# Kernel tuning notes

Hardware: AMD Instinct MI355X
Metric: run time of the kernel (lower is better)

Reference implementation:

```python
import jax, jax.numpy as jnp
import numpy as np

B, F, E = 4096, 39, 16
FIELD_DIMS = [1000] * F
OFFSETS = jnp.asarray(np.concatenate([[0], np.cumsum(FIELD_DIMS)[:-1]]).astype(np.int64))
I_IDX, J_IDX = np.triu_indices(F, 1)  # 741 pairs (i<j)
I_IDX = jnp.asarray(I_IDX); J_IDX = jnp.asarray(J_IDX)
MLP_DIMS = [2 * 741 * E, 400, 400, 400]
EPS = 1e-5


def setup_inputs() -> dict:
    key = jax.random.key(0)
    ks = jax.random.split(key, 20)
    s = 0.02
    inp = {
        'x': jax.random.randint(ks[0], (B, F), 0, 1000, dtype=jnp.int64),
        'emb': jax.random.normal(ks[1], (sum(FIELD_DIMS), E), jnp.float32) * s,
        'sen_w1': jax.random.normal(ks[2], (F, F), jnp.float32) * s,
        'sen_b1': jnp.zeros((F,), jnp.float32),
        'sen_w2': jax.random.normal(ks[3], (F, F), jnp.float32) * s,
        'sen_b2': jnp.zeros((F,), jnp.float32),
        'Wb1': jax.random.normal(ks[4], (E, E), jnp.float32) * s,
        'Wb2': jax.random.normal(ks[5], (E, E), jnp.float32) * s,
    }
    for li in range(3):
        din, dout = MLP_DIMS[li], MLP_DIMS[li + 1]
        inp[f'mw{li}'] = jax.random.normal(ks[6 + li], (dout, din), jnp.float32) * s
        inp[f'mb{li}'] = jnp.zeros((dout,), jnp.float32)
        inp[f'g{li}'] = jnp.ones((dout,), jnp.float32)
        inp[f'be{li}'] = jnp.zeros((dout,), jnp.float32)
    inp['mw3'] = jax.random.normal(ks[9], (1, MLP_DIMS[-1]), jnp.float32) * s
    inp['mb3'] = jnp.zeros((1,), jnp.float32)
    return inp


def _bilinear_all(v, W):
    # v: [B,F,E]; p_ij = (v_i W^T) * v_j for all i<j -> [B, P*E]
    proj = jnp.einsum('bfe,de->bfd', v, W)
    p = proj[:, I_IDX] * v[:, J_IDX]  # [B, 741, E]
    return p.reshape(v.shape[0], -1)


def _bn(h, g, be):
    mu = h.mean(axis=0)
    var = h.var(axis=0)
    return g * (h - mu) * jax.lax.rsqrt(var + EPS) + be


def _forward(x, emb, sen_w1, sen_b1, sen_w2, sen_b2, Wb1, Wb2,
             mw0, mb0, g0, be0, mw1, mb1, g1, be1, mw2, mb2, g2, be2, mw3, mb3):
    xe = emb[x + OFFSETS[None, :]]  # [B,F,E]
    # SENet: max over embed dim, two-layer excitation with ReLU
    z = jnp.max(xe, axis=2)  # [B,F]
    a = jax.nn.relu(jax.nn.relu(z @ sen_w1.T + sen_b1) @ sen_w2.T + sen_b2)  # [B,F]
    x_sen = a[:, :, None] * xe
    x_con = jnp.concatenate([_bilinear_all(xe, Wb1), _bilinear_all(x_sen, Wb2)], axis=1)
    h = x_con
    for w, b, g, be in ((mw0, mb0, g0, be0), (mw1, mb1, g1, be1), (mw2, mb2, g2, be2)):
        h = jax.nn.relu(_bn(h @ w.T + b, g, be))  # dropout = identity (eval)
    return h @ mw3.T + mb3  # [B,1]


def reference(x, emb, sen_w1, sen_b1, sen_w2, sen_b2, Wb1, Wb2,
              mw0, mb0, g0, be0, mw1, mb1, g1, be1, mw2, mb2, g2, be2, mw3, mb3):
    return _forward(x, emb, sen_w1, sen_b1, sen_w2, sen_b2, Wb1, Wb2,
                    mw0, mb0, g0, be0, mw1, mb1, g1, be1, mw2, mb2, g2, be2, mw3, mb3)
```

## Files before the change

### kernel.cpp

```cpp
#include <hip/hip_runtime.h>
#include <stdint.h>

#define B_ROWS  4096
#define F_FIELDS 39
#define NPAIR   741
#define XCON_K  23712
#define KP      23744
#define NP      512
#define HID     400
#define SPLITK0 8
#define KITERS0 (KP/64)

#define OFF_XCON 0ull
#define SZ_XCON  ((size_t)B_ROWS * KP * 2)
#define OFF_W0B  (OFF_XCON + SZ_XCON)
#define SZ_W0B   ((size_t)NP * KP * 2)
#define OFF_W1B  (OFF_W0B + SZ_W0B)
#define SZ_WSM   ((size_t)NP * NP * 2)
#define OFF_W2B  (OFF_W1B + SZ_WSM)
#define OFF_HPRE (OFF_W2B + SZ_WSM)
#define SZ_HPRE  ((size_t)B_ROWS * NP * 4)
#define OFF_HN   (OFF_HPRE + SZ_HPRE)
#define SZ_HN    ((size_t)B_ROWS * NP * 2)
#define OFF_STATS (OFF_HN + SZ_HN)
#define WS_NEEDED (OFF_STATS + 8192)

__device__ __forceinline__ unsigned short f2bf(float f) {
    union { float f; unsigned u; } v; v.f = f;
    unsigned r = (v.u + 0x7FFFu + ((v.u >> 16) & 1u)) >> 16;
    return (unsigned short)r;
}
__device__ __forceinline__ float bf2f(unsigned short h) {
    union { unsigned u; float f; } v; v.u = ((unsigned)h) << 16;
    return v.f;
}
__device__ __forceinline__ void gl_lds16(const void* g, void* l) {
    __builtin_amdgcn_global_load_lds(
        (const __attribute__((address_space(1))) void*)g,
        (__attribute__((address_space(3))) void*)l, 16, 0, 0);
}

typedef __bf16 bf16x8 __attribute__((ext_vector_type(8)));
typedef float  floatx4 __attribute__((ext_vector_type(4)));

__global__ __launch_bounds__(256) void build_xcon(
    const int* __restrict__ x, const float* __restrict__ emb,
    const float* __restrict__ w1, const float* __restrict__ b1,
    const float* __restrict__ w2, const float* __restrict__ b2,
    const float* __restrict__ Wb1, const float* __restrict__ Wb2,
    unsigned short* __restrict__ xcon)
{
    __shared__ float xe[624], pp[2][624];
    __shared__ float zz[40], tt[40], aa[40];
    __shared__ short itab[NPAIR], jtab[NPAIR];
    const int b = blockIdx.x, tid = threadIdx.x;

    for (int p = tid; p < NPAIR; p += 256) {
        int i = 0, s = 0;
        while (p >= s + (F_FIELDS - 1 - i)) { s += F_FIELDS - 1 - i; ++i; }
        itab[p] = (short)i;
        jtab[p] = (short)(i + 1 + (p - s));
    }
    if (tid < 156) {
        int f = tid >> 2, e4 = (tid & 3) * 4;
        int row = x[b * F_FIELDS + f] + 1000 * f;
        *(float4*)&xe[f * 16 + e4] = *(const float4*)&emb[row * 16 + e4];
    }
    __syncthreads();
    if (tid < F_FIELDS) {
        float m = xe[tid * 16];
        for (int e = 1; e < 16; ++e) m = fmaxf(m, xe[tid * 16 + e]);
        zz[tid] = m;
    }
    __syncthreads();
    if (tid < F_FIELDS) {
        float s = b1[tid];
        for (int g = 0; g < F_FIELDS; ++g) s += zz[g] * w1[tid * F_FIELDS + g];
        tt[tid] = fmaxf(s, 0.f);
    }
    __syncthreads();
    if (tid < F_FIELDS) {
        float s = b2[tid];
        for (int g = 0; g < F_FIELDS; ++g) s += tt[g] * w2[tid * F_FIELDS + g];
        aa[tid] = fmaxf(s, 0.f);
    }
    __syncthreads();
    for (int idx = tid; idx < 624; idx += 256) {
        int f = idx >> 4, d = idx & 15;
        float s1 = 0.f, s2 = 0.f;
        for (int e = 0; e < 16; ++e) {
            float v = xe[f * 16 + e];
            s1 += v * Wb1[d * 16 + e];
            s2 += v * Wb2[d * 16 + e];
        }
        pp[0][idx] = s1; pp[1][idx] = s2;
    }
    __syncthreads();
    unsigned short* out = xcon + (size_t)b * KP;
    for (int c = tid; c < 1484; c += 256) {
        if (c < 2 * NPAIR) {
            const int half = (c >= NPAIR);
            const int p = c - NPAIR * half;
            const int i = itab[p], j = jtab[p];
            const float f = half ? aa[i] * aa[j] : 1.f;
            const float* pr = &pp[half][i * 16];
            const float* xr = &xe[j * 16];
            unsigned short u[16];
#pragma unroll
            for (int e = 0; e < 16; ++e) u[e] = f2bf(f * pr[e] * xr[e]);
            uint4 v0, v1;
            v0.x = u[0] | ((unsigned)u[1] << 16);  v0.y = u[2] | ((unsigned)u[3] << 16);
            v0.z = u[4] | ((unsigned)u[5] << 16);  v0.w = u[6] | ((unsigned)u[7] << 16);
            v1.x = u[8] | ((unsigned)u[9] << 16);  v1.y = u[10] | ((unsigned)u[11] << 16);
            v1.z = u[12] | ((unsigned)u[13] << 16); v1.w = u[14] | ((unsigned)u[15] << 16);
            uint4* dst = (uint4*)(out + (half ? 11856 : 0) + p * 16);
            dst[0] = v0; dst[1] = v1;
        } else {
            uint4 z; z.x = z.y = z.z = z.w = 0u;
            ((uint4*)(out + XCON_K))[c - 2 * NPAIR] = z;
        }
    }
}

__global__ __launch_bounds__(256) void cvt_w0(const float* __restrict__ w, unsigned short* __restrict__ o_) {
    const int o = blockIdx.x;
    for (int k4 = threadIdx.x; k4 < KP / 4; k4 += 256) {
        const int k = k4 * 4;
        unsigned short u[4] = {0, 0, 0, 0};
        if (o < HID && k < XCON_K) {
            float4 v = *(const float4*)&w[(size_t)o * XCON_K + k];
            u[0] = f2bf(v.x); u[1] = f2bf(v.y); u[2] = f2bf(v.z); u[3] = f2bf(v.w);
        }
        uint2 pk; pk.x = u[0] | ((unsigned)u[1] << 16); pk.y = u[2] | ((unsigned)u[3] << 16);
        *(uint2*)&o_[(size_t)o * KP + k] = pk;
    }
}
__global__ __launch_bounds__(256) void cvt_wsm(const float* __restrict__ wa, const float* __restrict__ wb,
                                               unsigned short* __restrict__ oa, unsigned short* __restrict__ ob) {
    const int which = blockIdx.x >> 9;
    const int o = blockIdx.x & 511;
    const float* w = which ? wb : wa;
    unsigned short* o_ = which ? ob : oa;
    for (int k = threadIdx.x; k < NP; k += 256) {
        float v = (o < HID && k < HID) ? w[o * HID + k] : 0.f;
        o_[o * NP + k] = f2bf(v);
    }
}

__global__ __launch_bounds__(256, 2) void gemm0(
    const unsigned short* __restrict__ A, const unsigned short* __restrict__ Bm,
    float* __restrict__ C, int kcnt)
{
    __shared__ __align__(16) unsigned short As[128 * 64];
    __shared__ __align__(16) unsigned short Bs[256 * 64];
    const int tid = threadIdx.x;
    const int m0 = blockIdx.y * 128, n0 = blockIdx.x * 256;
    int kb = blockIdx.z * kcnt;
    int ke = kb + kcnt; if (ke > KITERS0) ke = KITERS0;

    const unsigned short* Ag = A + (size_t)(m0 + (tid >> 3)) * KP + ((tid & 7) * 8);
    const unsigned short* Bg = Bm + (size_t)(n0 + (tid >> 3)) * KP + ((tid & 7) * 8);
    unsigned short* Asl = As + tid * 8;
    unsigned short* Bsl = Bs + tid * 8;

    const int wv = tid >> 6, ln = tid & 63;
    const int wm = (wv >> 1) * 64, wn = (wv & 1) * 128;
    const int l15 = ln & 15, lq = ln >> 4;

    floatx4 acc[4][8];
#pragma unroll
    for (int mi = 0; mi < 4; ++mi)
#pragma unroll
        for (int ni = 0; ni < 8; ++ni)
            acc[mi][ni] = (floatx4){0.f, 0.f, 0.f, 0.f};

    for (int kt = kb; kt < ke; ++kt) {
        const size_t ko = (size_t)kt * 64;
#pragma unroll
        for (int i = 0; i < 4; ++i)
            gl_lds16(Ag + (size_t)(i * 32) * KP + ko, Asl + i * 2048);
#pragma unroll
        for (int i = 0; i < 8; ++i)
            gl_lds16(Bg + (size_t)(i * 32) * KP + ko, Bsl + i * 2048);
        __syncthreads();
#pragma unroll
        for (int kk = 0; kk < 64; kk += 32) {
            bf16x8 af[4], bfr[8];
#pragma unroll
            for (int t = 0; t < 4; ++t)
                af[t] = *(const bf16x8*)(As + (wm + t * 16 + l15) * 64 + kk + lq * 8);
#pragma unroll
            for (int t = 0; t < 8; ++t)
                bfr[t] = *(const bf16x8*)(Bs + (wn + t * 16 + l15) * 64 + kk + lq * 8);
#pragma unroll
            for (int mi = 0; mi < 4; ++mi)
#pragma unroll
                for (int ni = 0; ni < 8; ++ni)
                    acc[mi][ni] = __builtin_amdgcn_mfma_f32_16x16x32_bf16(
                        af[mi], bfr[ni], acc[mi][ni], 0, 0, 0);
        }
        __syncthreads();
    }
#pragma unroll
    for (int mi = 0; mi < 4; ++mi)
#pragma unroll
        for (int ni = 0; ni < 8; ++ni) {
            const int col = n0 + wn + ni * 16 + l15;
            const int row0 = m0 + wm + mi * 16 + lq * 4;
#pragma unroll
            for (int r = 0; r < 4; ++r)
                atomicAdd(&C[(size_t)(row0 + r) * NP + col], acc[mi][ni][r]);
        }
}

__global__ __launch_bounds__(256) void gemm_small(
    const unsigned short* __restrict__ A, const unsigned short* __restrict__ Bm,
    float* __restrict__ C)
{
    __shared__ __align__(16) unsigned short As[64 * 64];
    __shared__ __align__(16) unsigned short Bs[128 * 64];
    const int tid = threadIdx.x;
    const int m0 = blockIdx.y * 64, n0 = blockIdx.x * 128;

    const unsigned short* Ag = A + (size_t)(m0 + (tid >> 3)) * NP + ((tid & 7) * 8);
    const unsigned short* Bg = Bm + (size_t)(n0 + (tid >> 3)) * NP + ((tid & 7) * 8);
    unsigned short* Asl = As + tid * 8;
    unsigned short* Bsl = Bs + tid * 8;

    const int wv = tid >> 6, ln = tid & 63;
    const int wm = (wv >> 1) * 32, wn = (wv & 1) * 64;
    const int l15 = ln & 15, lq = ln >> 4;

    floatx4 acc[2][4];
#pragma unroll
    for (int mi = 0; mi < 2; ++mi)
#pragma unroll
        for (int ni = 0; ni < 4; ++ni)
            acc[mi][ni] = (floatx4){0.f, 0.f, 0.f, 0.f};

    for (int kt = 0; kt < NP / 64; ++kt) {
        const size_t ko = (size_t)kt * 64;
#pragma unroll
        for (int i = 0; i < 2; ++i)
            gl_lds16(Ag + (size_t)(i * 32) * NP + ko, Asl + i * 2048);
#pragma unroll
        for (int i = 0; i < 4; ++i)
            gl_lds16(Bg + (size_t)(i * 32) * NP + ko, Bsl + i * 2048);
        __syncthreads();
#pragma unroll
        for (int kk = 0; kk < 64; kk += 32) {
            bf16x8 af[2], bfr[4];
#pragma unroll
            for (int t = 0; t < 2; ++t)
                af[t] = *(const bf16x8*)(As + (wm + t * 16 + l15) * 64 + kk + lq * 8);
#pragma unroll
            for (int t = 0; t < 4; ++t)
                bfr[t] = *(const bf16x8*)(Bs + (wn + t * 16 + l15) * 64 + kk + lq * 8);
#pragma unroll
            for (int mi = 0; mi < 2; ++mi)
#pragma unroll
                for (int ni = 0; ni < 4; ++ni)
                    acc[mi][ni] = __builtin_amdgcn_mfma_f32_16x16x32_bf16(
                        af[mi], bfr[ni], acc[mi][ni], 0, 0, 0);
        }
        __syncthreads();
    }
#pragma unroll
    for (int mi = 0; mi < 2; ++mi)
#pragma unroll
        for (int ni = 0; ni < 4; ++ni) {
            const int col = n0 + wn + ni * 16 + l15;
            const int row0 = m0 + wm + mi * 16 + lq * 4;
#pragma unroll
            for (int r = 0; r < 4; ++r)
                C[(size_t)(row0 + r) * NP + col] = acc[mi][ni][r];
        }
}

__global__ __launch_bounds__(256) void colstats(const float* __restrict__ H,
                                                float* __restrict__ cs, float* __restrict__ csq) {
    const int tid = threadIdx.x;
    const int c4 = (tid & 127) * 4;
    const int ro = tid >> 7;
    const int r0 = blockIdx.x * 32;
    float s0 = 0, s1 = 0, s2 = 0, s3 = 0, q0 = 0, q1 = 0, q2 = 0, q3 = 0;
#pragma unroll
    for (int i = 0; i < 16; ++i) {
        float4 v = *(const float4*)&H[(size_t)(r0 + ro + 2 * i) * NP + c4];
        s0 += v.x; q0 += v.x * v.x;  s1 += v.y; q1 += v.y * v.y;
        s2 += v.z; q2 += v.z * v.z;  s3 += v.w; q3 += v.w * v.w;
    }
    atomicAdd(&cs[c4], s0); atomicAdd(&cs[c4 + 1], s1);
    atomicAdd(&cs[c4 + 2], s2); atomicAdd(&cs[c4 + 3], s3);
    atomicAdd(&csq[c4], q0); atomicAdd(&csq[c4 + 1], q1);
    atomicAdd(&csq[c4 + 2], q2); atomicAdd(&csq[c4 + 3], q3);
}

__global__ __launch_bounds__(256) void bnrelu(const float* __restrict__ H,
                       const float* __restrict__ cs, const float* __restrict__ csq,
                       const float* __restrict__ g, const float* __restrict__ be,
                       unsigned short* __restrict__ O) {
    __shared__ float sc[NP], sh[NP];
    for (int c = threadIdx.x; c < NP; c += 256) {
        float mean = cs[c] * (1.f / 4096.f);
        float var  = csq[c] * (1.f / 4096.f) - mean * mean;
        float s = (c < HID ? g[c] : 0.f) * rsqrtf(var + 1e-5f);
        sc[c] = s;
        sh[c] = (c < HID ? be[c] : 0.f) - mean * s;
    }
    __syncthreads();
    const size_t n4 = (size_t)B_ROWS * NP / 4;
    const size_t stride = (size_t)gridDim.x * 256;
    for (size_t i = (size_t)blockIdx.x * 256 + threadIdx.x; i < n4; i += stride) {
        const int c = (int)(i & 127) * 4;
        float4 v = ((const float4*)H)[i];
        unsigned short u0 = f2bf(fmaxf(v.x * sc[c]     + sh[c],     0.f));
        unsigned short u1 = f2bf(fmaxf(v.y * sc[c + 1] + sh[c + 1], 0.f));
        unsigned short u2 = f2bf(fmaxf(v.z * sc[c + 2] + sh[c + 2], 0.f));
        unsigned short u3 = f2bf(fmaxf(v.w * sc[c + 3] + sh[c + 3], 0.f));
        uint2 pk; pk.x = u0 | ((unsigned)u1 << 16); pk.y = u2 | ((unsigned)u3 << 16);
        *(uint2*)&O[i * 4] = pk;
    }
}

__global__ void final_dot(const unsigned short* __restrict__ H, const float* __restrict__ w,
                          const float* __restrict__ b, float* __restrict__ out) {
    const int row = blockIdx.x, ln = threadIdx.x;
    const unsigned short* h = H + (size_t)row * NP;
    float s = 0.f;
    for (int c = ln; c < HID; c += 64) s += bf2f(h[c]) * w[c];
    for (int o = 32; o; o >>= 1) s += __shfl_down(s, o);
    if (ln == 0) out[row] = s + b[0];
}

extern "C" void kernel_launch(void* const* d_in, const int* in_sizes, int n_in,
                              void* d_out, int out_size, void* d_ws, size_t ws_size,
                              hipStream_t stream)
{
    const int*   x    = (const int*)d_in[0];
    const float* emb  = (const float*)d_in[1];
    const float* sw1  = (const float*)d_in[2];
    const float* sb1  = (const float*)d_in[3];
    const float* sw2  = (const float*)d_in[4];
    const float* sb2  = (const float*)d_in[5];
    const float* Wb1  = (const float*)d_in[6];
    const float* Wb2  = (const float*)d_in[7];
    const float* mw0  = (const float*)d_in[8];
    const float* g0   = (const float*)d_in[10];
    const float* be0  = (const float*)d_in[11];
    const float* mw1  = (const float*)d_in[12];
    const float* g1   = (const float*)d_in[14];
    const float* be1  = (const float*)d_in[15];
    const float* mw2  = (const float*)d_in[16];
    const float* g2   = (const float*)d_in[18];
    const float* be2  = (const float*)d_in[19];
    const float* mw3  = (const float*)d_in[20];
    const float* mb3  = (const float*)d_in[21];
    (void)in_sizes; (void)n_in; (void)out_size;
    if (ws_size < WS_NEEDED) return;

    char* ws = (char*)d_ws;
    unsigned short* xcon = (unsigned short*)(ws + OFF_XCON);
    unsigned short* w0b  = (unsigned short*)(ws + OFF_W0B);
    unsigned short* w1b  = (unsigned short*)(ws + OFF_W1B);
    unsigned short* w2b  = (unsigned short*)(ws + OFF_W2B);
    float* hpre = (float*)(ws + OFF_HPRE);
    unsigned short* hn = (unsigned short*)(ws + OFF_HN);
    float* cs  = (float*)(ws + OFF_STATS);
    float* csq = cs + 512;

    build_xcon<<<B_ROWS, 256, 0, stream>>>(x, emb, sw1, sb1, sw2, sb2, Wb1, Wb2, xcon);
    cvt_w0<<<NP, 256, 0, stream>>>(mw0, w0b);
    cvt_wsm<<<2 * NP, 256, 0, stream>>>(mw1, mw2, w1b, w2b);

    hipMemsetAsync(hpre, 0, SZ_HPRE, stream);
    gemm0<<<dim3(NP / 256, B_ROWS / 128, SPLITK0), 256, 0, stream>>>(
        xcon, w0b, hpre, (KITERS0 + SPLITK0 - 1) / SPLITK0);

    auto bn = [&](const float* g, const float* be) {
        hipMemsetAsync(cs, 0, 4096, stream);
        colstats<<<128, 256, 0, stream>>>(hpre, cs, csq);
        bnrelu<<<512, 256, 0, stream>>>(hpre, cs, csq, g, be, hn);
    };
    bn(g0, be0);
    gemm_small<<<dim3(NP / 128, B_ROWS / 64), 256, 0, stream>>>(hn, w1b, hpre);
    bn(g1, be1);
    gemm_small<<<dim3(NP / 128, B_ROWS / 64), 256, 0, stream>>>(hn, w2b, hpre);
    bn(g2, be2);
    final_dot<<<B_ROWS, 64, 0, stream>>>(hn, mw3, mb3, (float*)d_out);
}
```

Before: 469.6 us.

## Shrink GEMM tiles, fuse final BN-ReLU with output dot, closed-form pair index

```diff
diff --git a/kernel.cpp b/kernel.cpp
--- a/kernel.cpp
+++ b/kernel.cpp
@@ -56,10 +56,12 @@
     const int b = blockIdx.x, tid = threadIdx.x;
 
     for (int p = tid; p < NPAIR; p += 256) {
-        int i = 0, s = 0;
-        while (p >= s + (F_FIELDS - 1 - i)) { s += F_FIELDS - 1 - i; ++i; }
+        float fp = (float)p;
+        int i = (int)(38.5f - sqrtf(38.5f * 38.5f - 2.f * fp));
+        while (i > 0 && p < (i * (77 - i)) / 2) --i;
+        while (p >= ((i + 1) * (76 - i)) / 2) ++i;
         itab[p] = (short)i;
-        jtab[p] = (short)(i + 1 + (p - s));
+        jtab[p] = (short)(i + 1 + (p - (i * (77 - i)) / 2));
     }
     if (tid < 156) {
         int f = tid >> 2, e4 = (tid & 3) * 4;
@@ -147,14 +149,14 @@
     }
 }
 
-__global__ __launch_bounds__(256, 2) void gemm0(
+__global__ __launch_bounds__(256, 4) void gemm0(
     const unsigned short* __restrict__ A, const unsigned short* __restrict__ Bm,
     float* __restrict__ C, int kcnt)
 {
-    __shared__ __align__(16) unsigned short As[128 * 64];
+    __shared__ __align__(16) unsigned short As[64 * 64];
     __shared__ __align__(16) unsigned short Bs[256 * 64];
     const int tid = threadIdx.x;
-    const int m0 = blockIdx.y * 128, n0 = blockIdx.x * 256;
+    const int m0 = blockIdx.y * 64, n0 = blockIdx.x * 256;
     int kb = blockIdx.z * kcnt;
     int ke = kb + kcnt; if (ke > KITERS0) ke = KITERS0;
 
@@ -164,12 +166,12 @@
     unsigned short* Bsl = Bs + tid * 8;
 
     const int wv = tid >> 6, ln = tid & 63;
-    const int wm = (wv >> 1) * 64, wn = (wv & 1) * 128;
+    const int wm = (wv >> 1) * 32, wn = (wv & 1) * 128;
     const int l15 = ln & 15, lq = ln >> 4;
 
-    floatx4 acc[4][8];
-#pragma unroll
-    for (int mi = 0; mi < 4; ++mi)
+    floatx4 acc[2][8];
+#pragma unroll
+    for (int mi = 0; mi < 2; ++mi)
 #pragma unroll
         for (int ni = 0; ni < 8; ++ni)
             acc[mi][ni] = (floatx4){0.f, 0.f, 0.f, 0.f};
@@ -177,7 +179,7 @@
     for (int kt = kb; kt < ke; ++kt) {
         const size_t ko = (size_t)kt * 64;
 #pragma unroll
-        for (int i = 0; i < 4; ++i)
+        for (int i = 0; i < 2; ++i)
             gl_lds16(Ag + (size_t)(i * 32) * KP + ko, Asl + i * 2048);
 #pragma unroll
         for (int i = 0; i < 8; ++i)
@@ -185,15 +187,15 @@
         __syncthreads();
 #pragma unroll
         for (int kk = 0; kk < 64; kk += 32) {
-            bf16x8 af[4], bfr[8];
-#pragma unroll
-            for (int t = 0; t < 4; ++t)
+            bf16x8 af[2], bfr[8];
+#pragma unroll
+            for (int t = 0; t < 2; ++t)
                 af[t] = *(const bf16x8*)(As + (wm + t * 16 + l15) * 64 + kk + lq * 8);
 #pragma unroll
             for (int t = 0; t < 8; ++t)
                 bfr[t] = *(const bf16x8*)(Bs + (wn + t * 16 + l15) * 64 + kk + lq * 8);
 #pragma unroll
-            for (int mi = 0; mi < 4; ++mi)
+            for (int mi = 0; mi < 2; ++mi)
 #pragma unroll
                 for (int ni = 0; ni < 8; ++ni)
                     acc[mi][ni] = __builtin_amdgcn_mfma_f32_16x16x32_bf16(
@@ -202,7 +204,7 @@
         __syncthreads();
     }
 #pragma unroll
-    for (int mi = 0; mi < 4; ++mi)
+    for (int mi = 0; mi < 2; ++mi)
 #pragma unroll
         for (int ni = 0; ni < 8; ++ni) {
             const int col = n0 + wn + ni * 16 + l15;
@@ -218,9 +220,9 @@
     float* __restrict__ C)
 {
     __shared__ __align__(16) unsigned short As[64 * 64];
-    __shared__ __align__(16) unsigned short Bs[128 * 64];
+    __shared__ __align__(16) unsigned short Bs[64 * 64];
     const int tid = threadIdx.x;
-    const int m0 = blockIdx.y * 64, n0 = blockIdx.x * 128;
+    const int m0 = blockIdx.y * 64, n0 = blockIdx.x * 64;
 
     const unsigned short* Ag = A + (size_t)(m0 + (tid >> 3)) * NP + ((tid & 7) * 8);
     const unsigned short* Bg = Bm + (size_t)(n0 + (tid >> 3)) * NP + ((tid & 7) * 8);
@@ -228,38 +230,36 @@
     unsigned short* Bsl = Bs + tid * 8;
 
     const int wv = tid >> 6, ln = tid & 63;
-    const int wm = (wv >> 1) * 32, wn = (wv & 1) * 64;
+    const int wm = (wv >> 1) * 32, wn = (wv & 1) * 32;
     const int l15 = ln & 15, lq = ln >> 4;
 
-    floatx4 acc[2][4];
+    floatx4 acc[2][2];
 #pragma unroll
     for (int mi = 0; mi < 2; ++mi)
 #pragma unroll
-        for (int ni = 0; ni < 4; ++ni)
+        for (int ni = 0; ni < 2; ++ni)
             acc[mi][ni] = (floatx4){0.f, 0.f, 0.f, 0.f};
 
     for (int kt = 0; kt < NP / 64; ++kt) {
         const size_t ko = (size_t)kt * 64;
 #pragma unroll
-        for (int i = 0; i < 2; ++i)
+        for (int i = 0; i < 2; ++i) {
             gl_lds16(Ag + (size_t)(i * 32) * NP + ko, Asl + i * 2048);
-#pragma unroll
-        for (int i = 0; i < 4; ++i)
             gl_lds16(Bg + (size_t)(i * 32) * NP + ko, Bsl + i * 2048);
+        }
         __syncthreads();
 #pragma unroll
         for (int kk = 0; kk < 64; kk += 32) {
-            bf16x8 af[2], bfr[4];
-#pragma unroll
-            for (int t = 0; t < 2; ++t)
-                af[t] = *(const bf16x8*)(As + (wm + t * 16 + l15) * 64 + kk + lq * 8);
-#pragma unroll
-            for (int t = 0; t < 4; ++t)
+            bf16x8 af[2], bfr[2];
+#pragma unroll
+            for (int t = 0; t < 2; ++t) {
+                af[t]  = *(const bf16x8*)(As + (wm + t * 16 + l15) * 64 + kk + lq * 8);
                 bfr[t] = *(const bf16x8*)(Bs + (wn + t * 16 + l15) * 64 + kk + lq * 8);
+            }
 #pragma unroll
             for (int mi = 0; mi < 2; ++mi)
 #pragma unroll
-                for (int ni = 0; ni < 4; ++ni)
+                for (int ni = 0; ni < 2; ++ni)
                     acc[mi][ni] = __builtin_amdgcn_mfma_f32_16x16x32_bf16(
                         af[mi], bfr[ni], acc[mi][ni], 0, 0, 0);
         }
@@ -268,7 +268,7 @@
 #pragma unroll
     for (int mi = 0; mi < 2; ++mi)
 #pragma unroll
-        for (int ni = 0; ni < 4; ++ni) {
+        for (int ni = 0; ni < 2; ++ni) {
             const int col = n0 + wn + ni * 16 + l15;
             const int row0 = m0 + wm + mi * 16 + lq * 4;
 #pragma unroll
@@ -323,14 +323,40 @@
     }
 }
 
-__global__ void final_dot(const unsigned short* __restrict__ H, const float* __restrict__ w,
-                          const float* __restrict__ b, float* __restrict__ out) {
-    const int row = blockIdx.x, ln = threadIdx.x;
-    const unsigned short* h = H + (size_t)row * NP;
-    float s = 0.f;
-    for (int c = ln; c < HID; c += 64) s += bf2f(h[c]) * w[c];
-    for (int o = 32; o; o >>= 1) s += __shfl_down(s, o);
-    if (ln == 0) out[row] = s + b[0];
+__global__ __launch_bounds__(256) void bnrelu_dot(const float* __restrict__ H,
+                       const float* __restrict__ cs, const float* __restrict__ csq,
+                       const float* __restrict__ g, const float* __restrict__ be,
+                       const float* __restrict__ w3, const float* __restrict__ b3,
+                       float* __restrict__ out) {
+    __shared__ float sc[NP], sh[NP], ww[NP];
+    for (int c = threadIdx.x; c < NP; c += 256) {
+        float mean = cs[c] * (1.f / 4096.f);
+        float var  = csq[c] * (1.f / 4096.f) - mean * mean;
+        float s = (c < HID ? g[c] : 0.f) * rsqrtf(var + 1e-5f);
+        sc[c] = s;
+        sh[c] = (c < HID ? be[c] : 0.f) - mean * s;
+        ww[c] = (c < HID ? w3[c] : 0.f);
+    }
+    __syncthreads();
+    const float b0 = b3[0];
+    const int ln = threadIdx.x & 63;
+    const size_t n4 = (size_t)B_ROWS * NP / 4;
+    const size_t stride = (size_t)gridDim.x * 256;
+    for (size_t i = (size_t)blockIdx.x * 256 + threadIdx.x; i < n4; i += stride) {
+        const int c = (int)(i & 127) * 4;
+        const int row = (int)(i >> 7);
+        float4 v = ((const float4*)H)[i];
+        float s = fmaxf(v.x * sc[c]     + sh[c],     0.f) * ww[c]
+                + fmaxf(v.y * sc[c + 1] + sh[c + 1], 0.f) * ww[c + 1]
+                + fmaxf(v.z * sc[c + 2] + sh[c + 2], 0.f) * ww[c + 2]
+                + fmaxf(v.w * sc[c + 3] + sh[c + 3], 0.f) * ww[c + 3];
+#pragma unroll
+        for (int o = 32; o; o >>= 1) s += __shfl_down(s, o);
+        if (ln == 0) {
+            if ((i & 127) == 0) s += b0;
+            atomicAdd(&out[row], s);
+        }
+    }
 }
 
 extern "C" void kernel_launch(void* const* d_in, const int* in_sizes, int n_in,
@@ -374,7 +400,7 @@
     cvt_wsm<<<2 * NP, 256, 0, stream>>>(mw1, mw2, w1b, w2b);
 
     hipMemsetAsync(hpre, 0, SZ_HPRE, stream);
-    gemm0<<<dim3(NP / 256, B_ROWS / 128, SPLITK0), 256, 0, stream>>>(
+    gemm0<<<dim3(NP / 256, B_ROWS / 64, SPLITK0), 256, 0, stream>>>(
         xcon, w0b, hpre, (KITERS0 + SPLITK0 - 1) / SPLITK0);
 
     auto bn = [&](const float* g, const float* be) {
@@ -383,9 +409,11 @@
         bnrelu<<<512, 256, 0, stream>>>(hpre, cs, csq, g, be, hn);
     };
     bn(g0, be0);
-    gemm_small<<<dim3(NP / 128, B_ROWS / 64), 256, 0, stream>>>(hn, w1b, hpre);
+    gemm_small<<<dim3(NP / 64, B_ROWS / 64), 256, 0, stream>>>(hn, w1b, hpre);
     bn(g1, be1);
-    gemm_small<<<dim3(NP / 128, B_ROWS / 64), 256, 0, stream>>>(hn, w2b, hpre);
-    bn(g2, be2);
-    final_dot<<<B_ROWS, 64, 0, stream>>>(hn, mw3, mb3, (float*)d_out);
-}
+    gemm_small<<<dim3(NP / 64, B_ROWS / 64), 256, 0, stream>>>(hn, w2b, hpre);
+    hipMemsetAsync(cs, 0, 4096, stream);
+    colstats<<<128, 256, 0, stream>>>(hpre, cs, csq);
+    hipMemsetAsync(d_out, 0, (size_t)B_ROWS * 4, stream);
+    bnrelu_dot<<<512, 256, 0, stream>>>(hpre, cs, csq, g2, be2, mw3, mb3, (float*)d_out);
+}
```

Result: slower. 483.9 us (+3.1%).
